# Kernel tuning notes

Measured on AMD Instinct MI355X. Metric: run time of the kernel, lower is better.

## Reference

```python
import jax, jax.numpy as jnp
import numpy as np

EMBED_DIM = 512
NUM_HEADS = 8
D_HEAD = EMBED_DIM // NUM_HEADS  # 64
BLOCK = 64
SEQ = 8192
BATCH = 2
N_GLOBAL = 2
N_WINDOW = 3
N_RANDOM = 3
NB = SEQ // BLOCK  # 128 blocks
M = N_GLOBAL + N_WINDOW + N_RANDOM  # gathered key blocks per query block


def setup_inputs() -> dict:
    key = jax.random.key(0)
    ks = jax.random.split(key, 12)
    s = 0.05  # ~xavier scale for [512,64]
    return {
        "query": jax.random.normal(ks[0], (SEQ, BATCH, EMBED_DIM), jnp.float32),
        "key_inp": jax.random.normal(ks[1], (SEQ, BATCH, EMBED_DIM), jnp.float32),
        "value": jax.random.normal(ks[2], (SEQ, BATCH, EMBED_DIM), jnp.float32),
        "q_w": jax.random.normal(ks[3], (NUM_HEADS, EMBED_DIM, D_HEAD), jnp.float32) * s,
        "k_w": jax.random.normal(ks[4], (NUM_HEADS, EMBED_DIM, D_HEAD), jnp.float32) * s,
        "v_w": jax.random.normal(ks[5], (NUM_HEADS, EMBED_DIM, D_HEAD), jnp.float32) * s,
        "q_b": jnp.zeros((NUM_HEADS, D_HEAD), jnp.float32),
        "k_b": jnp.zeros((NUM_HEADS, D_HEAD), jnp.float32),
        "v_b": jnp.zeros((NUM_HEADS, D_HEAD), jnp.float32),
        "out_w": jax.random.normal(ks[6], (EMBED_DIM, EMBED_DIM), jnp.float32) * 0.04,
        "out_b": jnp.zeros((EMBED_DIM,), jnp.float32),
        "rand_idx": jax.random.randint(ks[7], (NB, N_RANDOM), 0, NB, dtype=jnp.int32),
    }


def _gather_block_idx(rand_idx):
    # per query block: global blocks + sliding window (mod NB) + random blocks -> [NB, M]
    glob = jnp.broadcast_to(jnp.arange(N_GLOBAL, dtype=jnp.int32), (NB, N_GLOBAL))
    half = N_WINDOW // 2
    win = (jnp.arange(NB, dtype=jnp.int32)[:, None]
           + jnp.arange(N_WINDOW, dtype=jnp.int32)[None, :] - half) % NB
    return jnp.concatenate([glob, win, rand_idx], axis=1)


def _sparse_attn(Q, K, V, rand_idx):
    # Q,K,V: [B,H,S,dh] -> out [B,H,S,dh]
    B, H, S, dh = Q.shape
    Qb = Q.reshape(B, H, NB, BLOCK, dh)
    Kb = K.reshape(B, H, NB, BLOCK, dh)
    Vb = V.reshape(B, H, NB, BLOCK, dh)
    idx = _gather_block_idx(rand_idx)              # [NB, M]
    Kg = Kb[:, :, idx]                              # [B,H,NB,M,BLOCK,dh]
    Vg = Vb[:, :, idx].reshape(B, H, NB, M * BLOCK, dh)
    scores = jnp.einsum('bhnqd,bhnmkd->bhnqmk', Qb, Kg) / jnp.sqrt(jnp.float32(dh))
    scores = scores.reshape(B, H, NB, BLOCK, M * BLOCK)
    attn = jax.nn.softmax(scores, axis=-1)
    out = jnp.einsum('bhnqk,bhnkd->bhnqd', attn, Vg)
    return out.reshape(B, H, S, dh)


def reference(query, key_inp, value, q_w, k_w, v_w, q_b, k_b, v_b, out_w, out_b, rand_idx):
    # batch_first=False: [S,B,E] -> [B,S,E]
    q = jnp.transpose(query, (1, 0, 2))
    k = jnp.transpose(key_inp, (1, 0, 2))
    v = jnp.transpose(value, (1, 0, 2))
    # per-head projections: [B,S,E] x [H,E,dh] -> [B,H,S,dh]
    Q = jnp.einsum('bse,hed->bhsd', q, q_w) + q_b[None, :, None, :]
    K = jnp.einsum('bse,hed->bhsd', k, k_w) + k_b[None, :, None, :]
    V = jnp.einsum('bse,hed->bhsd', v, v_w) + v_b[None, :, None, :]
    ao = _sparse_attn(Q, K, V, rand_idx)            # [B,H,S,dh]
    flat = jnp.transpose(ao, (0, 2, 1, 3)).reshape(BATCH * SEQ, EMBED_DIM)
    out = flat @ out_w.T + out_b                    # nn.Linear
    out = out.reshape(BATCH, SEQ, EMBED_DIM)
    return jnp.transpose(out, (1, 0, 2))            # back to [S,B,E]
```

## Files before the change

### kernel.cpp

```cpp
#include <hip/hip_runtime.h>
#include <stdint.h>

#define NBLK 128
#define KDIM 512

typedef __attribute__((ext_vector_type(8))) short short8;
typedef __attribute__((ext_vector_type(4))) float f32x4;
typedef unsigned short u16;

__device__ __forceinline__ u16 f2bf(float f) {
  unsigned u = __float_as_uint(f);
  u = u + 0x7fffu + ((u >> 16) & 1u);
  return (u16)(u >> 16);
}

__device__ __forceinline__ void g2l16(const void* g, void* l) {
  __builtin_amdgcn_global_load_lds(
      (__attribute__((address_space(1))) void*)(g),
      (__attribute__((address_space(3))) void*)(l), 16, 0, 0);
}

__global__ void conv_inputs(const float* __restrict__ q, const float* __restrict__ k,
                            const float* __restrict__ v, u16* __restrict__ qb,
                            u16* __restrict__ kb, u16* __restrict__ vb) {
  const float* src[3] = {q, k, v};
  u16* dst[3] = {qb, kb, vb};
  int t = blockIdx.x * 256 + threadIdx.x;
  int o = t * 4;
  int b = o >> 22;
  int s = (o >> 9) & 8191;
  int e = o & 511;
  float4 val = *(const float4*)(src[blockIdx.y] + ((s * 2 + b) * 512 + e));
  ushort4 r;
  r.x = f2bf(val.x); r.y = f2bf(val.y); r.z = f2bf(val.z); r.w = f2bf(val.w);
  *(ushort4*)(dst[blockIdx.y] + o) = r;
}

__global__ void prep_weights(const float* __restrict__ qw, const float* __restrict__ kw,
                             const float* __restrict__ vw, const float* __restrict__ ow,
                             u16* __restrict__ wqt, u16* __restrict__ wkt,
                             u16* __restrict__ wvt, u16* __restrict__ owb) {
  int t = blockIdx.x * 256 + threadIdx.x;
  int y = blockIdx.y;
  if (y < 3) {
    const float* w = (y == 0) ? qw : (y == 1) ? kw : vw;
    u16* dstp = (y == 0) ? wqt : (y == 1) ? wkt : wvt;
    int c = t >> 7;
    int e4 = (t & 127) * 4;
    int h = c >> 6, d = c & 63;
    const float* base = w + h * (512 * 64) + d;
    ushort4 r;
    r.x = f2bf(base[(e4 + 0) * 64]);
    r.y = f2bf(base[(e4 + 1) * 64]);
    r.z = f2bf(base[(e4 + 2) * 64]);
    r.w = f2bf(base[(e4 + 3) * 64]);
    *(ushort4*)(dstp + c * 512 + e4) = r;
  } else {
    float4 val = *(const float4*)(ow + t * 4);
    ushort4 r;
    r.x = f2bf(val.x); r.y = f2bf(val.y); r.z = f2bf(val.z); r.w = f2bf(val.w);
    *(ushort4*)(owb + t * 4) = r;
  }
}

template <int MODE>
__device__ __forceinline__ void gemm_core(const u16* __restrict__ A, const u16* __restrict__ BT,
                                          const float* __restrict__ bias, void* __restrict__ dstv,
                                          int tileM, int tileN, u16* sh) {
  const int t = threadIdx.x;
  const int lane = t & 63, w = t >> 6;
  const int l15 = lane & 15, quad = lane >> 4;
  const int wm = w >> 1, wn = w & 1;
  u16* As = sh;
  u16* Bs = sh + 4096;

  f32x4 acc[4][4];
#pragma unroll
  for (int i = 0; i < 4; ++i)
#pragma unroll
    for (int j = 0; j < 4; ++j) acc[i][j] = (f32x4){0.f, 0.f, 0.f, 0.f};

  const int s0 = t, s1 = t + 256;
  const int r0 = s0 >> 2, g0 = (s0 & 3) ^ (r0 & 3);
  const int r1 = s1 >> 2, g1 = (s1 & 3) ^ (r1 & 3);
  const u16* gA0 = A + (tileM + r0) * KDIM + g0 * 8;
  const u16* gA1 = A + (tileM + r1) * KDIM + g1 * 8;
  const u16* gB0 = BT + (tileN + r0) * KDIM + g0 * 8;
  const u16* gB1 = BT + (tileN + r1) * KDIM + g1 * 8;

  for (int k0 = 0; k0 < KDIM; k0 += 32) {
    __syncthreads();
    g2l16(gA0 + k0, As + s0 * 8);
    g2l16(gA1 + k0, As + s1 * 8);
    g2l16(gB0 + k0, Bs + s0 * 8);
    g2l16(gB1 + k0, Bs + s1 * 8);
    __syncthreads();
    short8 af[4], bf[4];
#pragma unroll
    for (int mt = 0; mt < 4; ++mt) {
      const int ra = wm * 64 + mt * 16 + l15;
      af[mt] = *(const short8*)(As + ra * 32 + ((quad ^ (ra & 3)) << 3));
    }
#pragma unroll
    for (int nt = 0; nt < 4; ++nt) {
      const int rb = wn * 64 + nt * 16 + l15;
      bf[nt] = *(const short8*)(Bs + rb * 32 + ((quad ^ (rb & 3)) << 3));
    }
#pragma unroll
    for (int mt = 0; mt < 4; ++mt)
#pragma unroll
      for (int nt = 0; nt < 4; ++nt)
        acc[mt][nt] = __builtin_amdgcn_mfma_f32_16x16x32_bf16(af[mt], bf[nt], acc[mt][nt], 0, 0, 0);
  }
  __syncthreads();

  if (MODE == 0 || MODE == 1) {
#pragma unroll
    for (int mt = 0; mt < 4; ++mt)
#pragma unroll
      for (int nt = 0; nt < 4; ++nt)
#pragma unroll
        for (int r = 0; r < 4; ++r) {
          const int lrow = wm * 64 + mt * 16 + quad * 4 + r;
          const int col = wn * 64 + nt * 16 + l15;
          float v = acc[mt][nt][r] + (MODE == 0 ? bias[tileN + col] : bias[tileM + lrow]);
          const int ch = col >> 3;
          sh[lrow * 128 + ((ch ^ (lrow & 7)) << 3) + (col & 7)] = f2bf(v);
        }
    __syncthreads();
#pragma unroll
    for (int p = 0; p < 8; ++p) {
      const int idx = p * 256 + t;
      const int row = idx >> 4, c = idx & 15;
      short8 vch = *(const short8*)(sh + row * 128 + ((c ^ (row & 7)) << 3));
      if (MODE == 0) {
        const int m = tileM + row, b = m >> 13, s = m & 8191;
        const int n0 = tileN + c * 8, h = n0 >> 6, d = n0 & 63;
        *(short8*)((u16*)dstv + (((b * 8 + h) * 8192 + s) * 64 + d)) = vch;
      } else {
        const int hd = tileM + row;
        const int n0 = tileN + c * 8, b = n0 >> 13, s = n0 & 8191;
        *(short8*)((u16*)dstv + ((b * 512 + hd) * 8192 + s)) = vch;
      }
    }
  } else {
    float* Cf = (float*)sh;
#pragma unroll
    for (int half = 0; half < 2; ++half) {
      if (wm == half) {
#pragma unroll
        for (int mt = 0; mt < 4; ++mt)
#pragma unroll
          for (int nt = 0; nt < 4; ++nt)
#pragma unroll
            for (int r = 0; r < 4; ++r) {
              const int lrow = mt * 16 + quad * 4 + r;
              const int col = wn * 64 + nt * 16 + l15;
              float v = acc[mt][nt][r] + bias[tileN + col];
              const int ch = col >> 2;
              Cf[lrow * 128 + ((ch ^ ((lrow & 7) << 2)) << 2) + (col & 3)] = v;
            }
      }
      __syncthreads();
#pragma unroll
      for (int p = 0; p < 8; ++p) {
        const int idx = p * 256 + t;
        const int row = idx >> 5, c = idx & 31;
        float4 v4 = *(const float4*)(Cf + row * 128 + ((c ^ ((row & 7) << 2)) << 2));
        const int m = tileM + half * 64 + row;
        const int s = m & 8191, b = m >> 13;
        *(float4*)((float*)dstv + ((s * 2 + b) * 512 + tileN + c * 4)) = v4;
      }
      __syncthreads();
    }
  }
}

__global__ __launch_bounds__(256, 3)
void gemm_qkv(const u16* __restrict__ qb, const u16* __restrict__ kb, const u16* __restrict__ vb,
              const u16* __restrict__ WqT, const u16* __restrict__ WkT, const u16* __restrict__ WvT,
              const float* __restrict__ qbi, const float* __restrict__ kbi, const float* __restrict__ vbi,
              u16* __restrict__ Qb, u16* __restrict__ Kb, u16* __restrict__ Vt) {
  __shared__ u16 sh[16384];
  const int id = blockIdx.x + blockIdx.y * 4;
  const int xs = (id >> 3) & 3;
  const int ys = (id & 7) * 16 + (id >> 5);
  const int z = blockIdx.z;
  if (z == 0)      gemm_core<0>(qb, WqT, qbi, Qb, ys * 128, xs * 128, sh);
  else if (z == 1) gemm_core<0>(kb, WkT, kbi, Kb, ys * 128, xs * 128, sh);
  else             gemm_core<1>(WvT, vb, vbi, Vt, xs * 128, ys * 128, sh);
}

__global__ __launch_bounds__(256, 3)
void gemm_out_k(const u16* __restrict__ AO, const u16* __restrict__ OW,
                const float* __restrict__ ob, float* __restrict__ out) {
  __shared__ u16 sh[16384];
  const int id = blockIdx.x + blockIdx.y * 4;
  const int xs = (id >> 3) & 3;
  const int ys = (id & 7) * 16 + (id >> 5);
  gemm_core<2>(AO, OW, ob, out, ys * 128, xs * 128, sh);
}

__global__ __launch_bounds__(256, 5)
void attn(const u16* __restrict__ Qb, const u16* __restrict__ Kb,
          const u16* __restrict__ Vt, const int* __restrict__ ridx,
          u16* __restrict__ AO) {
  __shared__ u16 Ks[64 * 64];
  __shared__ u16 Vs[64 * 64];
  __shared__ u16 Ps[64 * 64];
  const int blk = blockIdx.x;
  const int bh = blk & 15, nb = blk >> 4;
  const int b = bh >> 3, h = bh & 7;
  const int t = threadIdx.x, lane = t & 63, w = t >> 6;
  const int l15 = lane & 15, quad = lane >> 4;

  int bidx[8];
  bidx[0] = 0; bidx[1] = 1;
  bidx[2] = (nb + NBLK - 1) & (NBLK - 1);
  bidx[3] = nb;
  bidx[4] = (nb + 1) & (NBLK - 1);
  bidx[5] = ridx[nb * 3 + 0];
  bidx[6] = ridx[nb * 3 + 1];
  bidx[7] = ridx[nb * 3 + 2];

  const u16* qrow = Qb + (bh * 8192 + nb * 64 + w * 16 + l15) * 64;
  short8 aq0 = *(const short8*)(qrow + quad * 8);
  short8 aq1 = *(const short8*)(qrow + 32 + quad * 8);

  const int s0 = t, s1 = t + 256;
  const int r0 = s0 >> 3, c0 = (s0 & 7) ^ (r0 & 7);
  const int r1 = s1 >> 3, c1 = (s1 & 7) ^ (r1 & 7);
  const u16* Kbase = Kb + bh * 8192 * 64;
  const u16* Vbase = Vt + (bh * 64) * 8192;

  f32x4 oacc[4];
#pragma unroll
  for (int i = 0; i < 4; ++i) oacc[i] = (f32x4){0.f, 0.f, 0.f, 0.f};
  float lsum[4] = {0.f, 0.f, 0.f, 0.f};

  for (int m = 0; m < 8; ++m) {
    const int kb0 = bidx[m] * 64;
    __syncthreads();
    g2l16(Kbase + (kb0 + r0) * 64 + c0 * 8, Ks + s0 * 8);
    g2l16(Kbase + (kb0 + r1) * 64 + c1 * 8, Ks + s1 * 8);
    g2l16(Vbase + r0 * 8192 + kb0 + c0 * 8, Vs + s0 * 8);
    g2l16(Vbase + r1 * 8192 + kb0 + c1 * 8, Vs + s1 * 8);
    __syncthreads();

    f32x4 s[4];
#pragma unroll
    for (int i = 0; i < 4; ++i) s[i] = (f32x4){0.f, 0.f, 0.f, 0.f};
#pragma unroll
    for (int nt = 0; nt < 4; ++nt) {
      const int key = nt * 16 + l15;
      const u16* kr = Ks + key * 64;
      short8 bk0 = *(const short8*)(kr + ((quad ^ (key & 7)) << 3));
      short8 bk1 = *(const short8*)(kr + (((4 + quad) ^ (key & 7)) << 3));
      s[nt] = __builtin_amdgcn_mfma_f32_16x16x32_bf16(aq0, bk0, s[nt], 0, 0, 0);
      s[nt] = __builtin_amdgcn_mfma_f32_16x16x32_bf16(aq1, bk1, s[nt], 0, 0, 0);
    }

#pragma unroll
    for (int nt = 0; nt < 4; ++nt) {
      const int key = nt * 16 + l15;
      const int cp = key >> 3;
#pragma unroll
      for (int rr = 0; rr < 4; ++rr) {
        float p = __expf(s[nt][rr] * 0.125f);
        lsum[rr] += p;
        const int q = w * 16 + quad * 4 + rr;
        Ps[q * 64 + (((cp ^ (q & 7)) << 3) | (key & 7))] = f2bf(p);
      }
    }

    const int q2 = w * 16 + l15;
    const u16* pr = Ps + q2 * 64;
    short8 ap0 = *(const short8*)(pr + ((quad ^ (q2 & 7)) << 3));
    short8 ap1 = *(const short8*)(pr + (((4 + quad) ^ (q2 & 7)) << 3));
#pragma unroll
    for (int nt = 0; nt < 4; ++nt) {
      const int d = nt * 16 + l15;
      const u16* vr = Vs + d * 64;
      short8 bv0 = *(const short8*)(vr + ((quad ^ (d & 7)) << 3));
      short8 bv1 = *(const short8*)(vr + (((4 + quad) ^ (d & 7)) << 3));
      oacc[nt] = __builtin_amdgcn_mfma_f32_16x16x32_bf16(ap0, bv0, oacc[nt], 0, 0, 0);
      oacc[nt] = __builtin_amdgcn_mfma_f32_16x16x32_bf16(ap1, bv1, oacc[nt], 0, 0, 0);
    }
  }

#pragma unroll
  for (int msk = 1; msk < 16; msk <<= 1)
#pragma unroll
    for (int rr = 0; rr < 4; ++rr) lsum[rr] += __shfl_xor(lsum[rr], msk, 64);
  float inv[4];
#pragma unroll
  for (int rr = 0; rr < 4; ++rr) inv[rr] = __builtin_amdgcn_rcpf(lsum[rr]);

#pragma unroll
  for (int nt = 0; nt < 4; ++nt) {
    const int cc = h * 64 + nt * 16 + l15;
#pragma unroll
    for (int rr = 0; rr < 4; ++rr) {
      const int s = nb * 64 + w * 16 + quad * 4 + rr;
      AO[(b * 8192 + s) * 512 + cc] = f2bf(oacc[nt][rr] * inv[rr]);
    }
  }
}

extern "C" void kernel_launch(void* const* d_in, const int* in_sizes, int n_in,
                              void* d_out, int out_size, void* d_ws, size_t ws_size,
                              hipStream_t stream) {
  const float* q   = (const float*)d_in[0];
  const float* k   = (const float*)d_in[1];
  const float* v   = (const float*)d_in[2];
  const float* qw  = (const float*)d_in[3];
  const float* kw  = (const float*)d_in[4];
  const float* vw  = (const float*)d_in[5];
  const float* qbi = (const float*)d_in[6];
  const float* kbi = (const float*)d_in[7];
  const float* vbi = (const float*)d_in[8];
  const float* ow  = (const float*)d_in[9];
  const float* ob  = (const float*)d_in[10];
  const int*   ri  = (const int*)d_in[11];

  char* ws = (char*)d_ws;
  const size_t MB1 = 1024 * 1024;
  u16* qbuf = (u16*)(ws + 0);
  u16* kbuf = (u16*)(ws + 16 * MB1);
  u16* vbuf = (u16*)(ws + 32 * MB1);
  u16* AO   = (u16*)(ws + 0);
  u16* Qb   = (u16*)(ws + 48 * MB1);
  u16* Kb   = (u16*)(ws + 64 * MB1);
  u16* Vt   = (u16*)(ws + 80 * MB1);
  u16* WqT  = (u16*)(ws + 96 * MB1);
  u16* WkT  = (u16*)(ws + 96 * MB1 + 512 * 1024);
  u16* WvT  = (u16*)(ws + 97 * MB1);
  u16* OW   = (u16*)(ws + 97 * MB1 + 512 * 1024);

  conv_inputs<<<dim3(8192, 3), 256, 0, stream>>>(q, k, v, qbuf, kbuf, vbuf);
  prep_weights<<<dim3(256, 4), 256, 0, stream>>>(qw, kw, vw, ow, WqT, WkT, WvT, OW);
  gemm_qkv<<<dim3(4, 128, 3), 256, 0, stream>>>(qbuf, kbuf, vbuf, WqT, WkT, WvT,
                                                qbi, kbi, vbi, Qb, Kb, Vt);
  attn<<<2048, 256, 0, stream>>>(Qb, Kb, Vt, ri, AO);
  gemm_out_k<<<dim3(4, 128), 256, 0, stream>>>(AO, OW, ob, (float*)d_out);
}
```

Before: 252.4 us.

## Fuse fp32-to-bf16 input conversion into QKV GEMM with register-prefetched tiles

Removes the separate conv_inputs kernel. The QKV GEMM now reads the fp32 [S,B,E] activations directly and converts them to bf16 while staging them into LDS. The GEMM main loop changes from async global_load_lds to register prefetch: the next k-tile is loaded into registers during the MFMAs, then written to LDS with a new swizzle. This avoids a full write and re-read of the three bf16 input copies. In exchange, each QKV block reads twice as many bytes and uses more registers, and the launch bounds are raised to 4 blocks per SM.

```diff
diff --git a/kernel.cpp b/kernel.cpp
--- a/kernel.cpp
+++ b/kernel.cpp
@@ -14,26 +14,19 @@
   return (u16)(u >> 16);
 }
 
+__device__ __forceinline__ short8 pack8(float4 a, float4 b) {
+  short8 r;
+  r[0] = (short)f2bf(a.x); r[1] = (short)f2bf(a.y);
+  r[2] = (short)f2bf(a.z); r[3] = (short)f2bf(a.w);
+  r[4] = (short)f2bf(b.x); r[5] = (short)f2bf(b.y);
+  r[6] = (short)f2bf(b.z); r[7] = (short)f2bf(b.w);
+  return r;
+}
+
 __device__ __forceinline__ void g2l16(const void* g, void* l) {
   __builtin_amdgcn_global_load_lds(
       (__attribute__((address_space(1))) void*)(g),
       (__attribute__((address_space(3))) void*)(l), 16, 0, 0);
-}
-
-__global__ void conv_inputs(const float* __restrict__ q, const float* __restrict__ k,
-                            const float* __restrict__ v, u16* __restrict__ qb,
-                            u16* __restrict__ kb, u16* __restrict__ vb) {
-  const float* src[3] = {q, k, v};
-  u16* dst[3] = {qb, kb, vb};
-  int t = blockIdx.x * 256 + threadIdx.x;
-  int o = t * 4;
-  int b = o >> 22;
-  int s = (o >> 9) & 8191;
-  int e = o & 511;
-  float4 val = *(const float4*)(src[blockIdx.y] + ((s * 2 + b) * 512 + e));
-  ushort4 r;
-  r.x = f2bf(val.x); r.y = f2bf(val.y); r.z = f2bf(val.z); r.w = f2bf(val.w);
-  *(ushort4*)(dst[blockIdx.y] + o) = r;
 }
 
 __global__ void prep_weights(const float* __restrict__ qw, const float* __restrict__ kw,
@@ -63,8 +56,8 @@
   }
 }
 
-template <int MODE>
-__device__ __forceinline__ void gemm_core(const u16* __restrict__ A, const u16* __restrict__ BT,
+template <int MODE, bool AF32, bool BF32>
+__device__ __forceinline__ void gemm_core(const void* __restrict__ Av, const void* __restrict__ Bv,
                                           const float* __restrict__ bias, void* __restrict__ dstv,
                                           int tileM, int tileN, u16* sh) {
   const int t = threadIdx.x;
@@ -80,38 +73,111 @@
 #pragma unroll
     for (int j = 0; j < 4; ++j) acc[i][j] = (f32x4){0.f, 0.f, 0.f, 0.f};
 
-  const int s0 = t, s1 = t + 256;
-  const int r0 = s0 >> 2, g0 = (s0 & 3) ^ (r0 & 3);
-  const int r1 = s1 >> 2, g1 = (s1 & 3) ^ (r1 & 3);
-  const u16* gA0 = A + (tileM + r0) * KDIM + g0 * 8;
-  const u16* gA1 = A + (tileM + r1) * KDIM + g1 * 8;
-  const u16* gB0 = BT + (tileN + r0) * KDIM + g0 * 8;
-  const u16* gB1 = BT + (tileN + r1) * KDIM + g1 * 8;
+  const int r = t >> 1, h = t & 1;
+  const int swz = (r >> 1) & 3;
+
+  const float* gA32 = nullptr; const u16* gA16 = nullptr;
+  {
+    const int grow = tileM + r;
+    if (AF32) {
+      const int b = grow >> 13, s = grow & 8191;
+      gA32 = (const float*)Av + (size_t)(s * 2 + b) * 512 + h * 16;
+    } else {
+      gA16 = (const u16*)Av + (size_t)grow * 512 + h * 16;
+    }
+  }
+  const float* gB32 = nullptr; const u16* gB16 = nullptr;
+  {
+    const int grow = tileN + r;
+    if (BF32) {
+      const int b = grow >> 13, s = grow & 8191;
+      gB32 = (const float*)Bv + (size_t)(s * 2 + b) * 512 + h * 16;
+    } else {
+      gB16 = (const u16*)Bv + (size_t)grow * 512 + h * 16;
+    }
+  }
+
+  u16* ldsA = As + r * 32;
+  u16* ldsB = Bs + r * 32;
+  const int p0 = ((2 * h) ^ swz) << 3;
+  const int p1 = ((2 * h + 1) ^ swz) << 3;
+
+  float4 fa[4], fb[4];
+  short8 sa[2], sb[2];
+
+#define LOAD_TILE(k0)                                             \
+  do {                                                            \
+    if (AF32) {                                                   \
+      fa[0] = *(const float4*)(gA32 + (k0));                      \
+      fa[1] = *(const float4*)(gA32 + (k0) + 4);                  \
+      fa[2] = *(const float4*)(gA32 + (k0) + 8);                  \
+      fa[3] = *(const float4*)(gA32 + (k0) + 12);                 \
+    } else {                                                      \
+      sa[0] = *(const short8*)(gA16 + (k0));                      \
+      sa[1] = *(const short8*)(gA16 + (k0) + 8);                  \
+    }                                                             \
+    if (BF32) {                                                   \
+      fb[0] = *(const float4*)(gB32 + (k0));                      \
+      fb[1] = *(const float4*)(gB32 + (k0) + 4);                  \
+      fb[2] = *(const float4*)(gB32 + (k0) + 8);                  \
+      fb[3] = *(const float4*)(gB32 + (k0) + 12);                 \
+    } else {                                                      \
+      sb[0] = *(const short8*)(gB16 + (k0));                      \
+      sb[1] = *(const short8*)(gB16 + (k0) + 8);                  \
+    }                                                             \
+  } while (0)
+
+#define STORE_TILE()                                              \
+  do {                                                            \
+    if (AF32) {                                                   \
+      *(short8*)(ldsA + p0) = pack8(fa[0], fa[1]);                \
+      *(short8*)(ldsA + p1) = pack8(fa[2], fa[3]);                \
+    } else {                                                      \
+      *(short8*)(ldsA + p0) = sa[0];                              \
+      *(short8*)(ldsA + p1) = sa[1];                              \
+    }                                                             \
+    if (BF32) {                                                   \
+      *(short8*)(ldsB + p0) = pack8(fb[0], fb[1]);                \
+      *(short8*)(ldsB + p1) = pack8(fb[2], fb[3]);                \
+    } else {                                                      \
+      *(short8*)(ldsB + p0) = sb[0];                              \
+      *(short8*)(ldsB + p1) = sb[1];                              \
+    }                                                             \
+  } while (0)
+
+  LOAD_TILE(0);
+  STORE_TILE();
+  __syncthreads();
 
   for (int k0 = 0; k0 < KDIM; k0 += 32) {
-    __syncthreads();
-    g2l16(gA0 + k0, As + s0 * 8);
-    g2l16(gA1 + k0, As + s1 * 8);
-    g2l16(gB0 + k0, Bs + s0 * 8);
-    g2l16(gB1 + k0, Bs + s1 * 8);
-    __syncthreads();
+    const bool has_next = (k0 + 32 < KDIM);
+    if (has_next) LOAD_TILE(k0 + 32);
+
     short8 af[4], bf[4];
 #pragma unroll
     for (int mt = 0; mt < 4; ++mt) {
       const int ra = wm * 64 + mt * 16 + l15;
-      af[mt] = *(const short8*)(As + ra * 32 + ((quad ^ (ra & 3)) << 3));
+      af[mt] = *(const short8*)(As + ra * 32 + ((quad ^ ((ra >> 1) & 3)) << 3));
     }
 #pragma unroll
     for (int nt = 0; nt < 4; ++nt) {
       const int rb = wn * 64 + nt * 16 + l15;
-      bf[nt] = *(const short8*)(Bs + rb * 32 + ((quad ^ (rb & 3)) << 3));
+      bf[nt] = *(const short8*)(Bs + rb * 32 + ((quad ^ ((rb >> 1) & 3)) << 3));
     }
 #pragma unroll
     for (int mt = 0; mt < 4; ++mt)
 #pragma unroll
       for (int nt = 0; nt < 4; ++nt)
         acc[mt][nt] = __builtin_amdgcn_mfma_f32_16x16x32_bf16(af[mt], bf[nt], acc[mt][nt], 0, 0, 0);
-  }
+
+    if (has_next) {
+      __syncthreads();
+      STORE_TILE();
+      __syncthreads();
+    }
+  }
+#undef LOAD_TILE
+#undef STORE_TILE
   __syncthreads();
 
   if (MODE == 0 || MODE == 1) {
@@ -120,10 +186,10 @@
 #pragma unroll
       for (int nt = 0; nt < 4; ++nt)
 #pragma unroll
-        for (int r = 0; r < 4; ++r) {
-          const int lrow = wm * 64 + mt * 16 + quad * 4 + r;
+        for (int rr = 0; rr < 4; ++rr) {
+          const int lrow = wm * 64 + mt * 16 + quad * 4 + rr;
           const int col = wn * 64 + nt * 16 + l15;
-          float v = acc[mt][nt][r] + (MODE == 0 ? bias[tileN + col] : bias[tileM + lrow]);
+          float v = acc[mt][nt][rr] + (MODE == 0 ? bias[tileN + col] : bias[tileM + lrow]);
           const int ch = col >> 3;
           sh[lrow * 128 + ((ch ^ (lrow & 7)) << 3) + (col & 7)] = f2bf(v);
         }
@@ -135,8 +201,8 @@
       short8 vch = *(const short8*)(sh + row * 128 + ((c ^ (row & 7)) << 3));
       if (MODE == 0) {
         const int m = tileM + row, b = m >> 13, s = m & 8191;
-        const int n0 = tileN + c * 8, h = n0 >> 6, d = n0 & 63;
-        *(short8*)((u16*)dstv + (((b * 8 + h) * 8192 + s) * 64 + d)) = vch;
+        const int n0 = tileN + c * 8, hh = n0 >> 6, d = n0 & 63;
+        *(short8*)((u16*)dstv + (((b * 8 + hh) * 8192 + s) * 64 + d)) = vch;
       } else {
         const int hd = tileM + row;
         const int n0 = tileN + c * 8, b = n0 >> 13, s = n0 & 8191;
@@ -153,10 +219,10 @@
 #pragma unroll
           for (int nt = 0; nt < 4; ++nt)
 #pragma unroll
-            for (int r = 0; r < 4; ++r) {
-              const int lrow = mt * 16 + quad * 4 + r;
+            for (int rr = 0; rr < 4; ++rr) {
+              const int lrow = mt * 16 + quad * 4 + rr;
               const int col = wn * 64 + nt * 16 + l15;
-              float v = acc[mt][nt][r] + bias[tileN + col];
+              float v = acc[mt][nt][rr] + bias[tileN + col];
               const int ch = col >> 2;
               Cf[lrow * 128 + ((ch ^ ((lrow & 7) << 2)) << 2) + (col & 3)] = v;
             }
@@ -176,8 +242,8 @@
   }
 }
 
-__global__ __launch_bounds__(256, 3)
-void gemm_qkv(const u16* __restrict__ qb, const u16* __restrict__ kb, const u16* __restrict__ vb,
+__global__ __launch_bounds__(256, 4)
+void gemm_qkv(const float* __restrict__ q, const float* __restrict__ k, const float* __restrict__ v,
               const u16* __restrict__ WqT, const u16* __restrict__ WkT, const u16* __restrict__ WvT,
               const float* __restrict__ qbi, const float* __restrict__ kbi, const float* __restrict__ vbi,
               u16* __restrict__ Qb, u16* __restrict__ Kb, u16* __restrict__ Vt) {
@@ -186,19 +252,19 @@
   const int xs = (id >> 3) & 3;
   const int ys = (id & 7) * 16 + (id >> 5);
   const int z = blockIdx.z;
-  if (z == 0)      gemm_core<0>(qb, WqT, qbi, Qb, ys * 128, xs * 128, sh);
-  else if (z == 1) gemm_core<0>(kb, WkT, kbi, Kb, ys * 128, xs * 128, sh);
-  else             gemm_core<1>(WvT, vb, vbi, Vt, xs * 128, ys * 128, sh);
-}
-
-__global__ __launch_bounds__(256, 3)
+  if (z == 0)      gemm_core<0, true, false>(q, WqT, qbi, Qb, ys * 128, xs * 128, sh);
+  else if (z == 1) gemm_core<0, true, false>(k, WkT, kbi, Kb, ys * 128, xs * 128, sh);
+  else             gemm_core<1, false, true>(WvT, v, vbi, Vt, xs * 128, ys * 128, sh);
+}
+
+__global__ __launch_bounds__(256, 4)
 void gemm_out_k(const u16* __restrict__ AO, const u16* __restrict__ OW,
                 const float* __restrict__ ob, float* __restrict__ out) {
   __shared__ u16 sh[16384];
   const int id = blockIdx.x + blockIdx.y * 4;
   const int xs = (id >> 3) & 3;
   const int ys = (id & 7) * 16 + (id >> 5);
-  gemm_core<2>(AO, OW, ob, out, ys * 128, xs * 128, sh);
+  gemm_core<2, false, false>(AO, OW, ob, out, ys * 128, xs * 128, sh);
 }
 
 __global__ __launch_bounds__(256, 5)
@@ -325,21 +391,17 @@
 
   char* ws = (char*)d_ws;
   const size_t MB1 = 1024 * 1024;
-  u16* qbuf = (u16*)(ws + 0);
-  u16* kbuf = (u16*)(ws + 16 * MB1);
-  u16* vbuf = (u16*)(ws + 32 * MB1);
-  u16* AO   = (u16*)(ws + 0);
-  u16* Qb   = (u16*)(ws + 48 * MB1);
-  u16* Kb   = (u16*)(ws + 64 * MB1);
-  u16* Vt   = (u16*)(ws + 80 * MB1);
-  u16* WqT  = (u16*)(ws + 96 * MB1);
-  u16* WkT  = (u16*)(ws + 96 * MB1 + 512 * 1024);
-  u16* WvT  = (u16*)(ws + 97 * MB1);
-  u16* OW   = (u16*)(ws + 97 * MB1 + 512 * 1024);
-
-  conv_inputs<<<dim3(8192, 3), 256, 0, stream>>>(q, k, v, qbuf, kbuf, vbuf);
+  u16* Qb   = (u16*)(ws + 0);
+  u16* Kb   = (u16*)(ws + 16 * MB1);
+  u16* Vt   = (u16*)(ws + 32 * MB1);
+  u16* AO   = (u16*)(ws + 48 * MB1);
+  u16* WqT  = (u16*)(ws + 64 * MB1);
+  u16* WkT  = (u16*)(ws + 64 * MB1 + 512 * 1024);
+  u16* WvT  = (u16*)(ws + 65 * MB1);
+  u16* OW   = (u16*)(ws + 65 * MB1 + 512 * 1024);
+
   prep_weights<<<dim3(256, 4), 256, 0, stream>>>(qw, kw, vw, ow, WqT, WkT, WvT, OW);
-  gemm_qkv<<<dim3(4, 128, 3), 256, 0, stream>>>(qbuf, kbuf, vbuf, WqT, WkT, WvT,
+  gemm_qkv<<<dim3(4, 128, 3), 256, 0, stream>>>(q, k, v, WqT, WkT, WvT,
                                                 qbi, kbi, vbi, Qb, Kb, Vt);
   attn<<<2048, 256, 0, stream>>>(Qb, Kb, Vt, ri, AO);
   gemm_out_k<<<dim3(4, 128), 256, 0, stream>>>(AO, OW, ob, (float*)d_out);
```

Result: no change. 254.3 us (+0.7%).
